# Optimization experiments

Measured on AMD Instinct MI355X. Metric: run time of the kernel, lower is better.

## Reference

```python
import jax, jax.numpy as jnp
import numpy as np

B, S, D = 8, 512, 768
H_IMG, W_IMG, STRIDE = 1024, 768, 8


def setup_inputs() -> dict:
    key = jax.random.key(0)
    k1, k2, k3, k4, k5 = jax.random.split(key, 5)
    emb = jax.random.normal(k1, (B, S, D), dtype=jnp.float32)
    # word-level boxes, each word spans 2 tokens (tests the mean-aggregation path)
    nw = S // 2
    x0 = jax.random.randint(k2, (B, nw), 0, W_IMG - 80)
    y0 = jax.random.randint(k3, (B, nw), 0, H_IMG - 40)
    bw = jax.random.randint(k4, (B, nw), 8, 80)
    bh = jax.random.randint(k5, (B, nw), 8, 40)
    word_coors = jnp.stack([x0, y0, x0 + bw, y0 + bh], axis=-1).astype(jnp.int32)
    coors = jnp.repeat(word_coors, 2, axis=1)  # [B, S, 4] (x0, y0, x1, y1)
    # mask: valid tokens then padding (original code breaks at first mask==0)
    mask = (jnp.arange(S) < S - 64).astype(jnp.int32)
    mask = jnp.broadcast_to(mask, (B, S))
    return {"bert_embeddings": emb, "coors": coors, "mask": mask,
            "image_h": H_IMG, "image_w": W_IMG, "stride": STRIDE}


def _grid_one(emb, coors, mask, R, C, stride):
    # emb: [S, D], coors: [S, 4] int, mask: [S] int
    Sl, Dl = emb.shape
    valid = jnp.cumprod(mask) > 0  # tokens before the first mask==0
    same_as_prev = jnp.all(coors[1:] == coors[:-1], axis=-1)
    new_word = jnp.concatenate([jnp.array([True]), ~same_as_prev]) & valid
    seg = jnp.cumsum(new_word.astype(jnp.int32)) - 1  # word id per token
    seg_ids = jnp.where(valid, seg, Sl)  # invalid tokens -> dump segment
    seg_sum = jax.ops.segment_sum(emb, seg_ids, num_segments=Sl + 1)  # [S+1, D]
    seg_cnt = jax.ops.segment_sum(jnp.ones((Sl,), emb.dtype), seg_ids, num_segments=Sl + 1)
    # Faithful to original: at a new-word token, the accumulated mean of the
    # PREVIOUS word is written into the CURRENT word's box (zeros for first word).
    prev = seg - 1
    prev_c = jnp.clip(prev, 0)
    val = jnp.where((prev >= 0)[:, None],
                    seg_sum[prev_c] / jnp.maximum(seg_cnt[prev_c], 1.0)[:, None],
                    0.0)  # [S, D]
    wc = coors // stride  # [S, 4]
    r = jnp.arange(R)
    c = jnp.arange(C)
    rowcov = (r[None, :] >= wc[:, 1:2]) & (r[None, :] < wc[:, 3:4])  # [S, R]
    colcov = (c[None, :] >= wc[:, 0:1]) & (c[None, :] < wc[:, 2:3])  # [S, C]
    cover = new_word[:, None, None] & rowcov[:, :, None] & colcov[:, None, :]  # [S, R, C]
    # later writes overwrite earlier ones -> take the last covering write per pixel
    idx = jnp.where(cover, jnp.arange(Sl)[:, None, None], -1)
    last = jnp.max(idx, axis=0)  # [R, C]
    grid = jnp.where((last >= 0)[:, :, None], val[jnp.clip(last, 0)], 0.0)  # [R, C, D]
    return jnp.transpose(grid, (2, 0, 1))  # [D, R, C]


def reference(bert_embeddings, coors, mask, image_h, image_w, stride):
    R = image_h // stride
    C = image_w // stride
    return jax.vmap(lambda e, co, m: _grid_one(e, co, m, R, C, stride))(
        bert_embeddings, coors, mask)
```

## Files before the change

### kernel.cpp

```cpp
#include <hip/hip_runtime.h>
#include <hip/hip_bf16.h>

constexpr int B_MAX  = 8;
constexpr int S      = 512;
constexpr int D      = 768;
constexpr int H_IMG  = 1024;
constexpr int W_IMG  = 768;
constexpr int STRIDE = 8;
constexpr int R  = H_IMG / STRIDE;
constexpr int C  = W_IMG / STRIDE;
constexpr int RC = R * C;

__global__ void seg_kernel(const int* __restrict__ coors,
                           const int* __restrict__ mask,
                           const int* __restrict__ stride_ptr,
                           int* __restrict__ wstart,
                           int* __restrict__ wcnt,
                           int* __restrict__ wbox,
                           int* __restrict__ nwords_arr) {
    const int b = blockIdx.x;
    const int t = threadIdx.x;

    __shared__ int s_nvalid;
    __shared__ int scan[S];
    __shared__ int sstart[S];

    if (t == 0) s_nvalid = S;
    __syncthreads();
    if (mask[b * S + t] == 0) atomicMin(&s_nvalid, t);
    __syncthreads();
    const int nv = s_nvalid;
    const bool valid = t < nv;

    const int4 c4 = *(const int4*)(coors + (size_t)(b * S + t) * 4);
    bool same = false;
    if (t > 0) {
        const int4 p4 = *(const int4*)(coors + (size_t)(b * S + t - 1) * 4);
        same = (c4.x == p4.x) && (c4.y == p4.y) && (c4.z == p4.z) && (c4.w == p4.w);
    }
    const int nw = (valid && (t == 0 || !same)) ? 1 : 0;

    scan[t] = nw;
    __syncthreads();
    for (int off = 1; off < S; off <<= 1) {
        int v = scan[t] + ((t >= off) ? scan[t - off] : 0);
        __syncthreads();
        scan[t] = v;
        __syncthreads();
    }

    const int stride = *stride_ptr;
    if (nw) {
        const int w = scan[t] - 1;
        sstart[w] = t;
        int* bx = wbox + ((size_t)b * S + w) * 4;
        bx[0] = c4.y / stride;
        bx[1] = c4.w / stride;
        bx[2] = c4.x / stride;
        bx[3] = c4.z / stride;
    }
    __syncthreads();

    const int NW = scan[S - 1];
    if (t == 0) nwords_arr[b] = NW;
    if (t < NW) {
        const int st  = sstart[t];
        const int nxt = (t + 1 < NW) ? sstart[t + 1] : nv;
        wstart[b * S + t] = st;
        wcnt[b * S + t]   = nxt - st;
    }
}

__global__ void mean_kernel(const float* __restrict__ emb,
                            const int* __restrict__ wstart,
                            const int* __restrict__ wcnt,
                            const int* __restrict__ nwords_arr,
                            float* __restrict__ valw) {
    const int bw = blockIdx.x;
    const int b  = bw / S;
    const int w  = bw % S;
    if (w >= nwords_arr[b]) return;

    float* out = valw + ((size_t)b * S + w) * D;
    if (w == 0) {
        for (int d = threadIdx.x; d < D; d += blockDim.x) out[d] = 0.0f;
        return;
    }
    const int pst  = wstart[b * S + w - 1];
    const int pcnt = wcnt[b * S + w - 1];
    const float inv = 1.0f / (float)max(pcnt, 1);
    const float* e0 = emb + ((size_t)b * S + pst) * D;
    for (int d = threadIdx.x; d < D; d += blockDim.x) {
        float s = 0.0f;
        for (int k = 0; k < pcnt; ++k) s += e0[(size_t)k * D + d];
        out[d] = s * inv;
    }
}

__global__ void init_last(int* __restrict__ last, int n) {
    int i = blockIdx.x * blockDim.x + threadIdx.x;
    if (i < n) last[i] = -1;
}

__global__ void paint_kernel(const int* __restrict__ wbox,
                             const int* __restrict__ nwords_arr,
                             int* __restrict__ last) {
    const int b = blockIdx.y;
    const int w = blockIdx.x;
    if (w >= nwords_arr[b]) return;
    const int* bx = wbox + ((size_t)b * S + w) * 4;
    const int r0 = max(bx[0], 0), r1 = min(bx[1], R);
    const int c0 = max(bx[2], 0), c1 = min(bx[3], C);
    const int nr = r1 - r0, nc = c1 - c0;
    if (nr <= 0 || nc <= 0) return;
    const int tot = nr * nc;
    for (int i = threadIdx.x; i < tot; i += blockDim.x) {
        const int r = r0 + i / nc;
        const int c = c0 + i % nc;
        atomicMax(&last[b * RC + r * C + c], w);
    }
}

__global__ void out_kernel(const float* __restrict__ valw,
                           const int* __restrict__ last,
                           float* __restrict__ out,
                           int Bv) {
    const size_t i = (size_t)blockIdx.x * blockDim.x + threadIdx.x;
    const size_t total = (size_t)Bv * D * (RC / 4);
    if (i >= total) return;
    const int    rc4 = (int)(i % (RC / 4));
    const size_t bd  = i / (RC / 4);
    const int    d   = (int)(bd % D);
    const int    b   = (int)(bd / D);

    const int4 l4 = ((const int4*)(last + (size_t)b * RC))[rc4];
    const float* vb = valw + (size_t)b * S * D + d;
    float4 o;
    o.x = (l4.x >= 0) ? vb[(size_t)l4.x * D] : 0.0f;
    o.y = (l4.y >= 0) ? vb[(size_t)l4.y * D] : 0.0f;
    o.z = (l4.z >= 0) ? vb[(size_t)l4.z * D] : 0.0f;
    o.w = (l4.w >= 0) ? vb[(size_t)l4.w * D] : 0.0f;
    ((float4*)out)[i] = o;
}

extern "C" void kernel_launch(void* const* d_in, const int* in_sizes, int n_in,
                              void* d_out, int out_size, void* d_ws, size_t ws_size,
                              hipStream_t stream) {
    const float* emb        = (const float*)d_in[0];
    const int*   coors      = (const int*)d_in[1];
    const int*   mask       = (const int*)d_in[2];
    const int*   stride_ptr = (const int*)d_in[5];
    float*       out        = (float*)d_out;

    const int Bv = in_sizes[2] / S;

    float* valw   = (float*)d_ws;
    int*   last   = (int*)(valw + (size_t)Bv * S * D);
    int*   wstart = last + (size_t)Bv * RC;
    int*   wcnt   = wstart + (size_t)Bv * S;
    int*   wbox   = wcnt + (size_t)Bv * S;
    int*   nwords = wbox + (size_t)Bv * S * 4;

    seg_kernel<<<Bv, S, 0, stream>>>(coors, mask, stride_ptr, wstart, wcnt, wbox, nwords);
    mean_kernel<<<Bv * S, 256, 0, stream>>>(emb, wstart, wcnt, nwords, valw);
    init_last<<<(Bv * RC + 255) / 256, 256, 0, stream>>>(last, Bv * RC);
    paint_kernel<<<dim3(S, Bv), 64, 0, stream>>>(wbox, nwords, last);

    const size_t total = (size_t)Bv * D * (RC / 4);
    out_kernel<<<(unsigned)((total + 255) / 256), 256, 0, stream>>>(valw, last, out, Bv);
}
```

Measured before the change: 339.8 us.

## Vectorize gather across channels, replace atomic painting with per-pixel scan

The output kernel now has each thread load float4 chunks of four channels for four pixels and transpose them in registers into four float4 stores. This cuts the number of scattered gather loads from the word-mean table. The init and atomic paint kernels are replaced by one kernel where each pixel scans all word boxes from shared memory and keeps the last one that covers it, removing atomics and one launch. The mean kernel is vectorized to float4 with a 2D grid. The trade-off is extra compute, since every pixel now loops over every word.

```diff
diff --git a/kernel.cpp b/kernel.cpp
--- a/kernel.cpp
+++ b/kernel.cpp
@@ -1,7 +1,6 @@
 #include <hip/hip_runtime.h>
 #include <hip/hip_bf16.h>
 
-constexpr int B_MAX  = 8;
 constexpr int S      = 512;
 constexpr int D      = 768;
 constexpr int H_IMG  = 1024;
@@ -76,71 +75,69 @@
                             const int* __restrict__ wcnt,
                             const int* __restrict__ nwords_arr,
                             float* __restrict__ valw) {
-    const int bw = blockIdx.x;
-    const int b  = bw / S;
-    const int w  = bw % S;
+    const int w = blockIdx.x;
+    const int b = blockIdx.y;
     if (w >= nwords_arr[b]) return;
 
-    float* out = valw + ((size_t)b * S + w) * D;
-    if (w == 0) {
-        for (int d = threadIdx.x; d < D; d += blockDim.x) out[d] = 0.0f;
-        return;
-    }
+    float4* out4 = (float4*)(valw + ((size_t)b * S + w) * D);
+    const int t = threadIdx.x;
+    if (w == 0) { out4[t] = make_float4(0.f, 0.f, 0.f, 0.f); return; }
+
     const int pst  = wstart[b * S + w - 1];
     const int pcnt = wcnt[b * S + w - 1];
     const float inv = 1.0f / (float)max(pcnt, 1);
-    const float* e0 = emb + ((size_t)b * S + pst) * D;
-    for (int d = threadIdx.x; d < D; d += blockDim.x) {
-        float s = 0.0f;
-        for (int k = 0; k < pcnt; ++k) s += e0[(size_t)k * D + d];
-        out[d] = s * inv;
+    const float4* e4 = (const float4*)(emb + ((size_t)b * S + pst) * D);
+    float4 s = make_float4(0.f, 0.f, 0.f, 0.f);
+    for (int k = 0; k < pcnt; ++k) {
+        float4 v = e4[(size_t)k * (D / 4) + t];
+        s.x += v.x; s.y += v.y; s.z += v.z; s.w += v.w;
     }
+    out4[t] = make_float4(s.x * inv, s.y * inv, s.z * inv, s.w * inv);
 }
 
-__global__ void init_last(int* __restrict__ last, int n) {
-    int i = blockIdx.x * blockDim.x + threadIdx.x;
-    if (i < n) last[i] = -1;
-}
+__global__ void last_kernel(const int* __restrict__ wbox,
+                            const int* __restrict__ nwords_arr,
+                            int* __restrict__ last) {
+    const int b  = blockIdx.y;
+    const int NW = nwords_arr[b];
 
-__global__ void paint_kernel(const int* __restrict__ wbox,
-                             const int* __restrict__ nwords_arr,
-                             int* __restrict__ last) {
-    const int b = blockIdx.y;
-    const int w = blockIdx.x;
-    if (w >= nwords_arr[b]) return;
-    const int* bx = wbox + ((size_t)b * S + w) * 4;
-    const int r0 = max(bx[0], 0), r1 = min(bx[1], R);
-    const int c0 = max(bx[2], 0), c1 = min(bx[3], C);
-    const int nr = r1 - r0, nc = c1 - c0;
-    if (nr <= 0 || nc <= 0) return;
-    const int tot = nr * nc;
-    for (int i = threadIdx.x; i < tot; i += blockDim.x) {
-        const int r = r0 + i / nc;
-        const int c = c0 + i % nc;
-        atomicMax(&last[b * RC + r * C + c], w);
+    __shared__ int4 sbox[S];
+    for (int i = threadIdx.x; i < NW; i += blockDim.x)
+        sbox[i] = ((const int4*)wbox)[b * S + i];
+    __syncthreads();
+
+    const int rc = blockIdx.x * blockDim.x + threadIdx.x;
+    const int r  = rc / C;
+    const int c  = rc % C;
+    int w = -1;
+    for (int i = 0; i < NW; ++i) {
+        const int4 bx = sbox[i];
+        if (r >= bx.x && r < bx.y && c >= bx.z && c < bx.w) w = i;
     }
+    last[b * RC + rc] = w;
 }
 
 __global__ void out_kernel(const float* __restrict__ valw,
                            const int* __restrict__ last,
-                           float* __restrict__ out,
-                           int Bv) {
-    const size_t i = (size_t)blockIdx.x * blockDim.x + threadIdx.x;
-    const size_t total = (size_t)Bv * D * (RC / 4);
-    if (i >= total) return;
-    const int    rc4 = (int)(i % (RC / 4));
-    const size_t bd  = i / (RC / 4);
-    const int    d   = (int)(bd % D);
-    const int    b   = (int)(bd / D);
+                           float* __restrict__ out) {
+    const int rc4 = blockIdx.x * blockDim.x + threadIdx.x;
+    const int d4  = blockIdx.y;
+    const int b   = blockIdx.z;
 
     const int4 l4 = ((const int4*)(last + (size_t)b * RC))[rc4];
-    const float* vb = valw + (size_t)b * S * D + d;
-    float4 o;
-    o.x = (l4.x >= 0) ? vb[(size_t)l4.x * D] : 0.0f;
-    o.y = (l4.y >= 0) ? vb[(size_t)l4.y * D] : 0.0f;
-    o.z = (l4.z >= 0) ? vb[(size_t)l4.z * D] : 0.0f;
-    o.w = (l4.w >= 0) ? vb[(size_t)l4.w * D] : 0.0f;
-    ((float4*)out)[i] = o;
+    const float* vb = valw + (size_t)b * S * D + d4 * 4;
+    const float4 z = make_float4(0.f, 0.f, 0.f, 0.f);
+    const float4 v0 = (l4.x >= 0) ? *(const float4*)(vb + (size_t)l4.x * D) : z;
+    const float4 v1 = (l4.y >= 0) ? *(const float4*)(vb + (size_t)l4.y * D) : z;
+    const float4 v2 = (l4.z >= 0) ? *(const float4*)(vb + (size_t)l4.z * D) : z;
+    const float4 v3 = (l4.w >= 0) ? *(const float4*)(vb + (size_t)l4.w * D) : z;
+
+    float4* ob = (float4*)(out + ((size_t)(b * D + d4 * 4)) * RC) + rc4;
+    constexpr int STRIDE4 = RC / 4;
+    ob[0]           = make_float4(v0.x, v1.x, v2.x, v3.x);
+    ob[STRIDE4]     = make_float4(v0.y, v1.y, v2.y, v3.y);
+    ob[2 * STRIDE4] = make_float4(v0.z, v1.z, v2.z, v3.z);
+    ob[3 * STRIDE4] = make_float4(v0.w, v1.w, v2.w, v3.w);
 }
 
 extern "C" void kernel_launch(void* const* d_in, const int* in_sizes, int n_in,
@@ -162,10 +159,7 @@
     int*   nwords = wbox + (size_t)Bv * S * 4;
 
     seg_kernel<<<Bv, S, 0, stream>>>(coors, mask, stride_ptr, wstart, wcnt, wbox, nwords);
-    mean_kernel<<<Bv * S, 256, 0, stream>>>(emb, wstart, wcnt, nwords, valw);
-    init_last<<<(Bv * RC + 255) / 256, 256, 0, stream>>>(last, Bv * RC);
-    paint_kernel<<<dim3(S, Bv), 64, 0, stream>>>(wbox, nwords, last);
-
-    const size_t total = (size_t)Bv * D * (RC / 4);
-    out_kernel<<<(unsigned)((total + 255) / 256), 256, 0, stream>>>(valw, last, out, Bv);
+    mean_kernel<<<dim3(S, Bv), D / 4, 0, stream>>>(emb, wstart, wcnt, nwords, valw);
+    last_kernel<<<dim3(RC / 256, Bv), 256, 0, stream>>>(wbox, nwords, last);
+    out_kernel<<<dim3(RC / 4 / 256, D / 4, Bv), 256, 0, stream>>>(valw, last, out);
 }
```

Result: slower. 366.4 us, median of 2 (+7.9%).
